# Performance work log

Measured on AMD Instinct MI355X. Metric: run time of the kernel, lower is better.

Reference implementation:

```python
import jax, jax.numpy as jnp
import numpy as np

C = 1024
H = 16
T = 2048
B = 2
EPS = 1e-5


def _layernorm(x, g, b):
    mu = jnp.mean(x, axis=-1, keepdims=True)
    var = jnp.mean(jnp.square(x - mu), axis=-1, keepdims=True)
    return (x - mu) * jax.lax.rsqrt(var + EPS) * g + b


def setup_inputs() -> dict:
    key = jax.random.key(0)
    ks = jax.random.split(key, 12)
    s = 1.0 / np.sqrt(C)
    inp = {
        "x": jax.random.normal(ks[0], (B, T, C), jnp.float32),
        "ln1_g": jnp.ones((C,), jnp.float32),
        "ln1_b": jnp.zeros((C,), jnp.float32),
        "Wq": jax.random.normal(ks[1], (C, C), jnp.float32) * s,
        "bq": jnp.zeros((C,), jnp.float32),
        "Wk": jax.random.normal(ks[2], (C, C), jnp.float32) * s,
        "bk": jnp.zeros((C,), jnp.float32),
        "Wv": jax.random.normal(ks[3], (C, C), jnp.float32) * s,
        "bv": jnp.zeros((C,), jnp.float32),
        "Wp": jax.random.normal(ks[4], (C, C), jnp.float32) * s,
        "bp": jnp.zeros((C,), jnp.float32),
        "ln2_g": jnp.ones((C,), jnp.float32),
        "ln2_b": jnp.zeros((C,), jnp.float32),
        "W1": jax.random.normal(ks[5], (C, 4 * C), jnp.float32) * s,
        "b1": jnp.zeros((4 * C,), jnp.float32),
        "W2": jax.random.normal(ks[6], (4 * C, C), jnp.float32) * (1.0 / np.sqrt(4 * C)),
        "b2": jnp.zeros((C,), jnp.float32),
    }
    return inp


def _block(x, ln1_g, ln1_b, Wq, bq, Wk, bk, Wv, bv, Wp, bp,
           ln2_g, ln2_b, W1, b1, W2, b2):
    b, t, c = x.shape
    hd = c // H
    h = _layernorm(x, ln1_g, ln1_b)
    q = (h @ Wq + bq).reshape(b, t, H, hd).transpose(0, 2, 1, 3)  # [B,H,T,hd]
    k = (h @ Wk + bk).reshape(b, t, H, hd).transpose(0, 2, 1, 3)
    v = (h @ Wv + bv).reshape(b, t, H, hd).transpose(0, 2, 1, 3)
    att = jnp.einsum("bhqd,bhkd->bhqk", q, k) * (1.0 / np.sqrt(hd))
    causal = jnp.tril(jnp.ones((t, t), bool))
    att = jnp.where(causal, att, -jnp.inf)
    att = jax.nn.softmax(att, axis=-1)
    y = jnp.einsum("bhqk,bhkd->bhqd", att, v)
    y = y.transpose(0, 2, 1, 3).reshape(b, t, c)
    x = x + (y @ Wp + bp)
    h2 = _layernorm(x, ln2_g, ln2_b)
    m = jax.nn.gelu(h2 @ W1 + b1, approximate=False)  # torch nn.GELU default = exact
    x = x + (m @ W2 + b2)
    return x


def reference(x, ln1_g, ln1_b, Wq, bq, Wk, bk, Wv, bv, Wp, bp,
              ln2_g, ln2_b, W1, b1, W2, b2):
    return _block(x, ln1_g, ln1_b, Wq, bq, Wk, bk, Wv, bv, Wp, bp,
                  ln2_g, ln2_b, W1, b1, W2, b2)
```

## Files before the change

### kernel.cpp

```cpp
#include <hip/hip_runtime.h>
#include <hip/hip_bf16.h>


#define TT 2048
#define CC 1024

typedef __attribute__((ext_vector_type(8))) short short8;
typedef __attribute__((ext_vector_type(4))) float floatx4;

__device__ __forceinline__ unsigned short f2bf(float f) {
    union { float f; unsigned u; } x; x.f = f;
    unsigned r = x.u + 0x7fff + ((x.u >> 16) & 1);
    return (unsigned short)(r >> 16);
}

__device__ __forceinline__ float fast_exp2(float x) {
#if __has_builtin(__builtin_amdgcn_exp2f)
    return __builtin_amdgcn_exp2f(x);
#else
    return exp2f(x);
#endif
}

__device__ __forceinline__ float fast_rcp(float x) {
#if __has_builtin(__builtin_amdgcn_rcpf)
    return __builtin_amdgcn_rcpf(x);
#else
    return 1.0f / x;
#endif
}

__device__ __forceinline__ float fast_gelu(float v) {
    float u = 0.79788456f * v + 0.035677408f * v * v * v;
    float e = fast_exp2(2.8853901f * u);
    return v - v * fast_rcp(e + 1.0f);
}

__device__ __forceinline__ void gld_lds16(const unsigned short* g, unsigned short* l) {
    __builtin_amdgcn_global_load_lds(
        (const __attribute__((address_space(1))) unsigned int*)g,
        (__attribute__((address_space(3))) unsigned int*)l, 16, 0, 0);
}

__global__ __launch_bounds__(256)
void prep_weights(const float* __restrict__ Wq, const float* __restrict__ Wk,
                  const float* __restrict__ Wv, const float* __restrict__ Wp,
                  const float* __restrict__ W1, const float* __restrict__ W2,
                  const float* __restrict__ bq, const float* __restrict__ bk,
                  const float* __restrict__ bv,
                  __hip_bfloat16* __restrict__ wqkvT, __hip_bfloat16* __restrict__ wpT,
                  __hip_bfloat16* __restrict__ w1T, __hip_bfloat16* __restrict__ w2T,
                  float* __restrict__ bqkv) {
    __shared__ float tile[32][33];
    int bid = blockIdx.x;
    int tid = threadIdx.x;
    if (bid >= 12288) {
#pragma unroll
        for (int it = 0; it < 12; ++it) {
            int i = it * 256 + tid;
            bqkv[i] = (i < 1024) ? bq[i] : (i < 2048) ? bk[i - 1024] : bv[i - 2048];
        }
        return;
    }
    const float* src; __hip_bfloat16* dst; int K, N, bxi, byi;
    if (bid < 4096) {
        int w = bid >> 10;
        src = (w == 0) ? Wq : (w == 1) ? Wk : (w == 2) ? Wv : Wp;
        dst = (w == 3) ? wpT : wqkvT + (size_t)w * 1024 * 1024;
        K = 1024; N = 1024;
        int r = bid & 1023; bxi = r & 31; byi = r >> 5;
    } else if (bid < 8192) {
        src = W1; dst = w1T; K = 1024; N = 4096;
        int r = bid - 4096; bxi = r & 127; byi = r >> 7;
    } else {
        src = W2; dst = w2T; K = 4096; N = 1024;
        int r = bid - 8192; bxi = r & 31; byi = r >> 5;
    }
    int tx = tid & 31, ty = tid >> 5;
    int n0 = bxi * 32, k0 = byi * 32;
#pragma unroll
    for (int i = 0; i < 4; ++i)
        tile[ty + i * 8][tx] = src[(size_t)(k0 + ty + i * 8) * N + n0 + tx];
    __syncthreads();
#pragma unroll
    for (int i = 0; i < 4; ++i)
        dst[(size_t)(n0 + ty + i * 8) * K + k0 + tx] = __float2bfloat16(tile[tx][ty + i * 8]);
}

__global__ __launch_bounds__(256)
void ln_kernel(const float* __restrict__ x, const float* __restrict__ g,
               const float* __restrict__ b, __hip_bfloat16* __restrict__ out) {
    int row = blockIdx.x;
    int tid = threadIdx.x;
    const float* xr = x + (size_t)row * CC;
    float4 v = *(const float4*)(xr + tid * 4);
    float s = v.x + v.y + v.z + v.w;
#pragma unroll
    for (int m = 1; m < 64; m <<= 1) s += __shfl_xor(s, m, 64);
    __shared__ float red[4], red2[4];
    int wv = tid >> 6;
    if ((tid & 63) == 0) red[wv] = s;
    __syncthreads();
    float mu = (red[0] + red[1] + red[2] + red[3]) * (1.0f / CC);
    float d0 = v.x - mu, d1 = v.y - mu, d2 = v.z - mu, d3 = v.w - mu;
    float s2 = d0 * d0 + d1 * d1 + d2 * d2 + d3 * d3;
#pragma unroll
    for (int m = 1; m < 64; m <<= 1) s2 += __shfl_xor(s2, m, 64);
    if ((tid & 63) == 0) red2[wv] = s2;
    __syncthreads();
    float var = (red2[0] + red2[1] + red2[2] + red2[3]) * (1.0f / CC);
    float rs = rsqrtf(var + 1e-5f);
    float4 gv = *(const float4*)(g + tid * 4);
    float4 bv = *(const float4*)(b + tid * 4);
    __hip_bfloat16* o = out + (size_t)row * CC + tid * 4;
    o[0] = __float2bfloat16(d0 * rs * gv.x + bv.x);
    o[1] = __float2bfloat16(d1 * rs * gv.y + bv.y);
    o[2] = __float2bfloat16(d2 * rs * gv.z + bv.z);
    o[3] = __float2bfloat16(d3 * rs * gv.w + bv.w);
}

#define BM 128
#define BK 64

template <int MODE, int TBN>
__global__ __launch_bounds__(256)
void gemm_bt(const unsigned short* __restrict__ A, const unsigned short* __restrict__ Bt,
             const float* __restrict__ bias, const float* __restrict__ res,
             void* __restrict__ out, unsigned short* __restrict__ vt,
             int M, int N, int K) {
    constexpr int IM = (TBN == 64) ? 2 : 4;
    __shared__ __align__(16) unsigned short As[BM * BK];
    __shared__ __align__(16) unsigned short Bs[TBN * BK];
    int tid = threadIdx.x;
    int lane = tid & 63;
    int wave = tid >> 6;
    int wm = (TBN == 64) ? wave * 32 : (wave >> 1) * 64;
    int wn = (TBN == 64) ? 0 : (wave & 1) * 64;
    int rowBase = blockIdx.x * BM;
    int colBase = blockIdx.y * TBN;
    int lr = lane & 15;
    int quad = lane >> 4;

    floatx4 acc[IM][4] = {};

    for (int k0 = 0; k0 < K; k0 += BK) {
#pragma unroll
        for (int hh = 0; hh < BM / 32; ++hh) {
            int s = tid + hh * 256;
            int r = s >> 3, p = s & 7;
            int c = p ^ (r & 7);
            gld_lds16(A + (size_t)(rowBase + r) * K + k0 + c * 8, As + (size_t)s * 8);
        }
#pragma unroll
        for (int hh = 0; hh < TBN / 32; ++hh) {
            int s = tid + hh * 256;
            int r = s >> 3, p = s & 7;
            int c = p ^ (r & 7);
            gld_lds16(Bt + (size_t)(colBase + r) * K + k0 + c * 8, Bs + (size_t)s * 8);
        }
        __syncthreads();
#pragma unroll
        for (int koi = 0; koi < 2; ++koi) {
            int ch = ((koi * 4 + quad) ^ (lr & 7)) * 8;
            short8 a[IM], b[4];
#pragma unroll
            for (int i = 0; i < IM; ++i)
                a[i] = *(const short8*)(As + (wm + i * 16 + lr) * BK + ch);
#pragma unroll
            for (int j = 0; j < 4; ++j)
                b[j] = *(const short8*)(Bs + (wn + j * 16 + lr) * BK + ch);
#pragma unroll
            for (int i = 0; i < IM; ++i)
#pragma unroll
                for (int j = 0; j < 4; ++j)
                    acc[i][j] = __builtin_amdgcn_mfma_f32_16x16x32_bf16(a[i], b[j], acc[i][j], 0, 0, 0);
        }
        __syncthreads();
    }

    if (MODE == 3 && colBase >= 2048) {
#pragma unroll
        for (int i = 0; i < IM; ++i) {
            int row0 = rowBase + wm + i * 16 + (lane >> 4) * 4;
            int bb = row0 >> 11, t0 = row0 & (TT - 1);
#pragma unroll
            for (int j = 0; j < 4; ++j) {
                int col = colBase + wn + j * 16 + (lane & 15);
                float bi = bias[col];
                int dg = col - 2048;
                int hh = dg >> 6, dd = dg & 63;
                ushort4 pk;
                pk.x = f2bf(acc[i][j][0] + bi);
                pk.y = f2bf(acc[i][j][1] + bi);
                pk.z = f2bf(acc[i][j][2] + bi);
                pk.w = f2bf(acc[i][j][3] + bi);
                *(ushort4*)(vt + ((size_t)(bb * 16 + hh) * 64 + dd) * TT + t0) = pk;
            }
        }
        return;
    }

    unsigned short* outb = (unsigned short*)out;
    float* outf = (float*)out;
#pragma unroll
    for (int i = 0; i < IM; ++i) {
        int row0 = rowBase + wm + i * 16 + (lane >> 4) * 4;
#pragma unroll
        for (int j = 0; j < 4; ++j) {
            int col = colBase + wn + j * 16 + (lane & 15);
            float bi = bias[col];
#pragma unroll
            for (int r = 0; r < 4; ++r) {
                size_t off = (size_t)(row0 + r) * N + col;
                float v = acc[i][j][r] + bi;
                if (MODE == 1) {
                    outf[off] = v + res[off];
                } else if (MODE == 2) {
                    outb[off] = f2bf(fast_gelu(v));
                } else {
                    outb[off] = f2bf(v);
                }
            }
        }
    }
}

__global__ __launch_bounds__(256)
void attn_mfma(const unsigned short* __restrict__ qkv,
               const unsigned short* __restrict__ vT,
               unsigned short* __restrict__ y) {
    __shared__ __align__(16) unsigned short Plds[4][32 * 72];
    __shared__ __align__(16) float cbuf[2][32][66];
    __shared__ float cltb[2][32];
    int wv = threadIdx.x >> 6, lane = threadIdx.x & 63;
    int quad = lane >> 4, l16 = lane & 15;
    int bx = blockIdx.x;
    int u = bx >> 5, bh = bx & 31;
    int t = wv >> 1, s = wv & 1;
    int qt = (31 - u) * 2 + t;
    int b = bh >> 4, h = bh & 15;

    const unsigned short* qb = qkv + (size_t)b * TT * 3072 + h * 64;
    const unsigned short* kb = qb + 1024;
    const unsigned short* vtb = vT + (size_t)bh * 64 * TT;
    unsigned short* Pw = Plds[wv];

    int q0 = qt * 32;
    short8 aq[2][2];
#pragma unroll
    for (int i = 0; i < 2; ++i)
#pragma unroll
        for (int c = 0; c < 2; ++c)
            aq[i][c] = *(const short8*)(qb + (size_t)(q0 + i * 16 + l16) * 3072 + c * 32 + quad * 8);

    short8 ones;
#pragma unroll
    for (int e = 0; e < 8; ++e) ones[e] = (short)0x3F80;

    floatx4 acc_o[2][4] = {};
    floatx4 lt[2] = {};

    const float k1 = 0.18033688f;
    const float k2 = 11.54156033f;

    int ntile = (qt >> 1) + 1;
    int nhalf = ntile >> 1;
    int ktbeg = s ? nhalf : 0;
    int ktend = s ? ntile : nhalf;

    for (int kt = ktbeg; kt < ktend; ++kt) {
        int k0 = kt * 64;
        short8 ck[4][2];
#pragma unroll
        for (int jt = 0; jt < 4; ++jt)
#pragma unroll
            for (int c = 0; c < 2; ++c)
                ck[jt][c] = *(const short8*)(kb + (size_t)(k0 + jt * 16 + l16) * 3072 + c * 32 + quad * 8);

        floatx4 sc[2][4] = {};
#pragma unroll
        for (int c = 0; c < 2; ++c)
#pragma unroll
            for (int i = 0; i < 2; ++i)
#pragma unroll
                for (int jt = 0; jt < 4; ++jt)
                    sc[i][jt] = __builtin_amdgcn_mfma_f32_16x16x32_bf16(aq[i][c], ck[jt][c], sc[i][jt], 0, 0, 0);

        if (kt == ntile - 1) {
#pragma unroll
            for (int i = 0; i < 2; ++i)
#pragma unroll
                for (int jt = 0; jt < 4; ++jt)
#pragma unroll
                    for (int r = 0; r < 4; ++r)
                        if (k0 + jt * 16 + l16 > q0 + i * 16 + quad * 4 + r) sc[i][jt][r] = -3.0e38f;
        }

#pragma unroll
        for (int i = 0; i < 2; ++i)
#pragma unroll
            for (int r = 0; r < 4; ++r) {
                int qrow = i * 16 + quad * 4 + r;
#pragma unroll
                for (int jt = 0; jt < 4; ++jt) {
                    float p = fast_exp2(fmaf(sc[i][jt][r], k1, -k2));
                    Pw[qrow * 72 + jt * 16 + l16] =
                        (unsigned short)(__float_as_uint(p) >> 16);
                }
            }

#pragma unroll
        for (int c = 0; c < 2; ++c) {
            short8 cv[4];
#pragma unroll
            for (int jd = 0; jd < 4; ++jd)
                cv[jd] = *(const short8*)(vtb + (size_t)(jd * 16 + l16) * TT + k0 + c * 32 + quad * 8);
#pragma unroll
            for (int i = 0; i < 2; ++i) {
                short8 ap = *(const short8*)(Pw + (i * 16 + l16) * 72 + c * 32 + quad * 8);
                lt[i] = __builtin_amdgcn_mfma_f32_16x16x32_bf16(ap, ones, lt[i], 0, 0, 0);
#pragma unroll
                for (int jd = 0; jd < 4; ++jd)
                    acc_o[i][jd] = __builtin_amdgcn_mfma_f32_16x16x32_bf16(ap, cv[jd], acc_o[i][jd], 0, 0, 0);
            }
        }
    }

    __syncthreads();
    if (s) {
#pragma unroll
        for (int i = 0; i < 2; ++i)
#pragma unroll
            for (int r = 0; r < 4; ++r) {
                int row = i * 16 + quad * 4 + r;
#pragma unroll
                for (int jd = 0; jd < 4; ++jd)
                    cbuf[t][row][jd * 16 + l16] = acc_o[i][jd][r];
                if (l16 == 0) cltb[t][row] = lt[i][r];
            }
    }
    __syncthreads();
    if (!s) {
#pragma unroll
        for (int i = 0; i < 2; ++i)
#pragma unroll
            for (int r = 0; r < 4; ++r) {
                int row = i * 16 + quad * 4 + r;
                float l2 = lt[i][r] + cltb[t][row];
                float rl = fast_rcp(l2);
                int grow = b * TT + q0 + row;
#pragma unroll
                for (int jd = 0; jd < 4; ++jd) {
                    float v = acc_o[i][jd][r] + cbuf[t][row][jd * 16 + l16];
                    y[(size_t)grow * CC + h * 64 + jd * 16 + l16] = f2bf(v * rl);
                }
            }
    }
}

extern "C" void kernel_launch(void* const* d_in, const int* in_sizes, int n_in,
                              void* d_out, int out_size, void* d_ws, size_t ws_size,
                              hipStream_t stream) {
    const float* x    = (const float*)d_in[0];
    const float* ln1g = (const float*)d_in[1];
    const float* ln1b = (const float*)d_in[2];
    const float* Wq   = (const float*)d_in[3];
    const float* bq   = (const float*)d_in[4];
    const float* Wk   = (const float*)d_in[5];
    const float* bk   = (const float*)d_in[6];
    const float* Wv   = (const float*)d_in[7];
    const float* bv   = (const float*)d_in[8];
    const float* Wp   = (const float*)d_in[9];
    const float* bp   = (const float*)d_in[10];
    const float* ln2g = (const float*)d_in[11];
    const float* ln2b = (const float*)d_in[12];
    const float* W1   = (const float*)d_in[13];
    const float* b1   = (const float*)d_in[14];
    const float* W2   = (const float*)d_in[15];
    const float* b2   = (const float*)d_in[16];

    const int M = 2 * TT;
    char* ws = (char*)d_ws;
    size_t off = 0;
    auto alloc = [&](size_t bytes) {
        char* p = ws + off;
        off += (bytes + 255) & ~(size_t)255;
        return p;
    };
    __hip_bfloat16* hb    = (__hip_bfloat16*)alloc((size_t)M * CC * 2);
    __hip_bfloat16* h2b   = (__hip_bfloat16*)alloc((size_t)M * CC * 2);
    unsigned short* yb    = (unsigned short*)alloc((size_t)M * CC * 2);
    __hip_bfloat16* wqkvT = (__hip_bfloat16*)alloc((size_t)3072 * CC * 2);
    __hip_bfloat16* wpT   = (__hip_bfloat16*)alloc((size_t)CC * CC * 2);
    __hip_bfloat16* w1T   = (__hip_bfloat16*)alloc((size_t)4096 * CC * 2);
    __hip_bfloat16* w2T   = (__hip_bfloat16*)alloc((size_t)CC * 4096 * 2);
    float*          bqkv  = (float*)alloc(3072 * 4);
    float*          x2    = (float*)alloc((size_t)M * CC * 4);
    unsigned short* qkv   = (unsigned short*)alloc((size_t)M * 3072 * 2);
    unsigned short* vT    = (unsigned short*)alloc((size_t)32 * 64 * TT * 2);
    unsigned short* mb    = (unsigned short*)alloc((size_t)M * 4096 * 2);
    (void)ws_size; (void)in_sizes; (void)n_in; (void)out_size;

    dim3 tb(256);
    prep_weights<<<12289, tb, 0, stream>>>(Wq, Wk, Wv, Wp, W1, W2, bq, bk, bv,
                                           wqkvT, wpT, w1T, w2T, bqkv);

    ln_kernel<<<M, 256, 0, stream>>>(x, ln1g, ln1b, hb);
    gemm_bt<3, 128><<<dim3(M / BM, 3072 / 128), tb, 0, stream>>>(
        (const unsigned short*)hb, (const unsigned short*)wqkvT, bqkv, nullptr, qkv, vT, M, 3072, 1024);
    attn_mfma<<<1024, tb, 0, stream>>>(qkv, vT, yb);
    gemm_bt<1, 64><<<dim3(M / BM, 1024 / 64), tb, 0, stream>>>(
        yb, (const unsigned short*)wpT, bp, x, x2, nullptr, M, 1024, 1024);
    ln_kernel<<<M, 256, 0, stream>>>(x2, ln2g, ln2b, h2b);
    gemm_bt<2, 128><<<dim3(M / BM, 4096 / 128), tb, 0, stream>>>(
        (const unsigned short*)h2b, (const unsigned short*)w1T, b1, nullptr, mb, nullptr, M, 4096, 1024);
    gemm_bt<1, 64><<<dim3(M / BM, 1024 / 64), tb, 0, stream>>>(
        mb, (const unsigned short*)w2T, b2, x2, (float*)d_out, nullptr, M, 1024, 4096);
}
```

Measured before the change: 378.6 us.

## Split attention key range across four waves per query tile, doubling grid

```diff
diff --git a/kernel.cpp b/kernel.cpp
--- a/kernel.cpp
+++ b/kernel.cpp
@@ -236,8 +236,8 @@
     int quad = lane >> 4, l16 = lane & 15;
     int bx = blockIdx.x;
     int u = bx >> 5, bh = bx & 31;
-    int t = wv >> 1, s = wv & 1;
-    int qt = (31 - u) * 2 + t;
+    int s = wv;
+    int qt = 63 - u;
     int b = bh >> 4, h = bh & 15;
 
     const unsigned short* qb = qkv + (size_t)b * TT * 3072 + h * 64;
@@ -264,9 +264,8 @@
     const float k2 = 11.54156033f;
 
     int ntile = (qt >> 1) + 1;
-    int nhalf = ntile >> 1;
-    int ktbeg = s ? nhalf : 0;
-    int ktend = s ? ntile : nhalf;
+    int ktbeg = (s * ntile) >> 2;
+    int ktend = ((s + 1) * ntile) >> 2;
 
     for (int kt = ktbeg; kt < ktend; ++kt) {
         int k0 = kt * 64;
@@ -327,7 +326,8 @@
     }
 
     __syncthreads();
-    if (s) {
+    if (s & 1) {
+        int cb = s >> 1;
 #pragma unroll
         for (int i = 0; i < 2; ++i)
 #pragma unroll
@@ -335,23 +335,50 @@
                 int row = i * 16 + quad * 4 + r;
 #pragma unroll
                 for (int jd = 0; jd < 4; ++jd)
-                    cbuf[t][row][jd * 16 + l16] = acc_o[i][jd][r];
-                if (l16 == 0) cltb[t][row] = lt[i][r];
-            }
-    }
-    __syncthreads();
-    if (!s) {
+                    cbuf[cb][row][jd * 16 + l16] = acc_o[i][jd][r];
+                if (l16 == 0) cltb[cb][row] = lt[i][r];
+            }
+    }
+    __syncthreads();
+    if (!(s & 1)) {
+        int cb = s >> 1;
 #pragma unroll
         for (int i = 0; i < 2; ++i)
 #pragma unroll
             for (int r = 0; r < 4; ++r) {
                 int row = i * 16 + quad * 4 + r;
-                float l2 = lt[i][r] + cltb[t][row];
+                lt[i][r] += cltb[cb][row];
+#pragma unroll
+                for (int jd = 0; jd < 4; ++jd)
+                    acc_o[i][jd][r] += cbuf[cb][row][jd * 16 + l16];
+            }
+    }
+    __syncthreads();
+    if (s == 2) {
+#pragma unroll
+        for (int i = 0; i < 2; ++i)
+#pragma unroll
+            for (int r = 0; r < 4; ++r) {
+                int row = i * 16 + quad * 4 + r;
+#pragma unroll
+                for (int jd = 0; jd < 4; ++jd)
+                    cbuf[0][row][jd * 16 + l16] = acc_o[i][jd][r];
+                if (l16 == 0) cltb[0][row] = lt[i][r];
+            }
+    }
+    __syncthreads();
+    if (s == 0) {
+#pragma unroll
+        for (int i = 0; i < 2; ++i)
+#pragma unroll
+            for (int r = 0; r < 4; ++r) {
+                int row = i * 16 + quad * 4 + r;
+                float l2 = lt[i][r] + cltb[0][row];
                 float rl = fast_rcp(l2);
                 int grow = b * TT + q0 + row;
 #pragma unroll
                 for (int jd = 0; jd < 4; ++jd) {
-                    float v = acc_o[i][jd][r] + cbuf[t][row][jd * 16 + l16];
+                    float v = acc_o[i][jd][r] + cbuf[0][row][jd * 16 + l16];
                     y[(size_t)grow * CC + h * 64 + jd * 16 + l16] = f2bf(v * rl);
                 }
             }
@@ -408,7 +435,7 @@
     ln_kernel<<<M, 256, 0, stream>>>(x, ln1g, ln1b, hb);
     gemm_bt<3, 128><<<dim3(M / BM, 3072 / 128), tb, 0, stream>>>(
         (const unsigned short*)hb, (const unsigned short*)wqkvT, bqkv, nullptr, qkv, vT, M, 3072, 1024);
-    attn_mfma<<<1024, tb, 0, stream>>>(qkv, vT, yb);
+    attn_mfma<<<2048, tb, 0, stream>>>(qkv, vT, yb);
     gemm_bt<1, 64><<<dim3(M / BM, 1024 / 64), tb, 0, stream>>>(
         yb, (const unsigned short*)wpT, bp, x, x2, nullptr, M, 1024, 1024);
     ln_kernel<<<M, 256, 0, stream>>>(x2, ln2g, ln2b, h2b);
```

Measured after the change: 378.8 us. Within noise of the previous version (+0.1%).

## Pair long and short causal query tiles per block to balance attention work

Applied to the files above, without the earlier changes.

```diff
diff --git a/kernel.cpp b/kernel.cpp
--- a/kernel.cpp
+++ b/kernel.cpp
@@ -236,98 +236,112 @@
     int quad = lane >> 4, l16 = lane & 15;
     int bx = blockIdx.x;
     int u = bx >> 5, bh = bx & 31;
-    int t = wv >> 1, s = wv & 1;
-    int qt = (31 - u) * 2 + t;
     int b = bh >> 4, h = bh & 15;
+    int qtA = 63 - u, qtB = u;
+    int nA = (qtA >> 1) + 1, nB = (qtB >> 1) + 1;
+
+    {
+        float* cz = &cbuf[0][0][0];
+        for (int i = threadIdx.x; i < 2 * 32 * 66; i += 256) cz[i] = 0.0f;
+        if (threadIdx.x < 64) (&cltb[0][0])[threadIdx.x] = 0.0f;
+    }
+    __syncthreads();
 
     const unsigned short* qb = qkv + (size_t)b * TT * 3072 + h * 64;
     const unsigned short* kb = qb + 1024;
     const unsigned short* vtb = vT + (size_t)bh * 64 * TT;
     unsigned short* Pw = Plds[wv];
 
-    int q0 = qt * 32;
-    short8 aq[2][2];
-#pragma unroll
-    for (int i = 0; i < 2; ++i)
-#pragma unroll
-        for (int c = 0; c < 2; ++c)
-            aq[i][c] = *(const short8*)(qb + (size_t)(q0 + i * 16 + l16) * 3072 + c * 32 + quad * 8);
-
     short8 ones;
 #pragma unroll
     for (int e = 0; e < 8; ++e) ones[e] = (short)0x3F80;
-
-    floatx4 acc_o[2][4] = {};
-    floatx4 lt[2] = {};
 
     const float k1 = 0.18033688f;
     const float k2 = 11.54156033f;
 
-    int ntile = (qt >> 1) + 1;
-    int nhalf = ntile >> 1;
-    int ktbeg = s ? nhalf : 0;
-    int ktend = s ? ntile : nhalf;
-
-    for (int kt = ktbeg; kt < ktend; ++kt) {
-        int k0 = kt * 64;
-        short8 ck[4][2];
-#pragma unroll
-        for (int jt = 0; jt < 4; ++jt)
+    int fbeg = (33 * wv) >> 2, fend = (33 * (wv + 1)) >> 2;
+
+    for (int seg = 0; seg < 2; ++seg) {
+        int t, sb, se;
+        if (seg == 0) {
+            if (fbeg < nA) { t = 0; sb = fbeg; se = (fend < nA) ? fend : nA; }
+            else           { t = 1; sb = fbeg - nA; se = fend - nA; }
+        } else {
+            if (fbeg < nA && fend > nA) { t = 1; sb = 0; se = fend - nA; }
+            else break;
+        }
+        int qt = t ? qtB : qtA;
+        int ntile = t ? nB : nA;
+        int q0 = qt * 32;
+
+        short8 aq[2][2];
+#pragma unroll
+        for (int i = 0; i < 2; ++i)
 #pragma unroll
             for (int c = 0; c < 2; ++c)
-                ck[jt][c] = *(const short8*)(kb + (size_t)(k0 + jt * 16 + l16) * 3072 + c * 32 + quad * 8);
-
-        floatx4 sc[2][4] = {};
-#pragma unroll
-        for (int c = 0; c < 2; ++c)
+                aq[i][c] = *(const short8*)(qb + (size_t)(q0 + i * 16 + l16) * 3072 + c * 32 + quad * 8);
+
+        floatx4 acc_o[2][4] = {};
+        floatx4 lt[2] = {};
+
+        for (int kt = sb; kt < se; ++kt) {
+            int k0 = kt * 64;
+            short8 ck[4][2];
+#pragma unroll
+            for (int jt = 0; jt < 4; ++jt)
+#pragma unroll
+                for (int c = 0; c < 2; ++c)
+                    ck[jt][c] = *(const short8*)(kb + (size_t)(k0 + jt * 16 + l16) * 3072 + c * 32 + quad * 8);
+
+            floatx4 sc[2][4] = {};
+#pragma unroll
+            for (int c = 0; c < 2; ++c)
+#pragma unroll
+                for (int i = 0; i < 2; ++i)
+#pragma unroll
+                    for (int jt = 0; jt < 4; ++jt)
+                        sc[i][jt] = __builtin_amdgcn_mfma_f32_16x16x32_bf16(aq[i][c], ck[jt][c], sc[i][jt], 0, 0, 0);
+
+            if (kt == ntile - 1) {
+#pragma unroll
+                for (int i = 0; i < 2; ++i)
+#pragma unroll
+                    for (int jt = 0; jt < 4; ++jt)
+#pragma unroll
+                        for (int r = 0; r < 4; ++r)
+                            if (k0 + jt * 16 + l16 > q0 + i * 16 + quad * 4 + r) sc[i][jt][r] = -3.0e38f;
+            }
+
 #pragma unroll
             for (int i = 0; i < 2; ++i)
 #pragma unroll
-                for (int jt = 0; jt < 4; ++jt)
-                    sc[i][jt] = __builtin_amdgcn_mfma_f32_16x16x32_bf16(aq[i][c], ck[jt][c], sc[i][jt], 0, 0, 0);
-
-        if (kt == ntile - 1) {
-#pragma unroll
-            for (int i = 0; i < 2; ++i)
-#pragma unroll
-                for (int jt = 0; jt < 4; ++jt)
-#pragma unroll
-                    for (int r = 0; r < 4; ++r)
-                        if (k0 + jt * 16 + l16 > q0 + i * 16 + quad * 4 + r) sc[i][jt][r] = -3.0e38f;
-        }
-
-#pragma unroll
-        for (int i = 0; i < 2; ++i)
-#pragma unroll
-            for (int r = 0; r < 4; ++r) {
-                int qrow = i * 16 + quad * 4 + r;
-#pragma unroll
-                for (int jt = 0; jt < 4; ++jt) {
-                    float p = fast_exp2(fmaf(sc[i][jt][r], k1, -k2));
-                    Pw[qrow * 72 + jt * 16 + l16] =
-                        (unsigned short)(__float_as_uint(p) >> 16);
+                for (int r = 0; r < 4; ++r) {
+                    int qrow = i * 16 + quad * 4 + r;
+#pragma unroll
+                    for (int jt = 0; jt < 4; ++jt) {
+                        float p = fast_exp2(fmaf(sc[i][jt][r], k1, -k2));
+                        Pw[qrow * 72 + jt * 16 + l16] =
+                            (unsigned short)(__float_as_uint(p) >> 16);
+                    }
                 }
-            }
-
-#pragma unroll
-        for (int c = 0; c < 2; ++c) {
-            short8 cv[4];
-#pragma unroll
-            for (int jd = 0; jd < 4; ++jd)
-                cv[jd] = *(const short8*)(vtb + (size_t)(jd * 16 + l16) * TT + k0 + c * 32 + quad * 8);
-#pragma unroll
-            for (int i = 0; i < 2; ++i) {
-                short8 ap = *(const short8*)(Pw + (i * 16 + l16) * 72 + c * 32 + quad * 8);
-                lt[i] = __builtin_amdgcn_mfma_f32_16x16x32_bf16(ap, ones, lt[i], 0, 0, 0);
+
+#pragma unroll
+            for (int c = 0; c < 2; ++c) {
+                short8 cv[4];
 #pragma unroll
                 for (int jd = 0; jd < 4; ++jd)
-                    acc_o[i][jd] = __builtin_amdgcn_mfma_f32_16x16x32_bf16(ap, cv[jd], acc_o[i][jd], 0, 0, 0);
-            }
-        }
-    }
-
-    __syncthreads();
-    if (s) {
+                    cv[jd] = *(const short8*)(vtb + (size_t)(jd * 16 + l16) * TT + k0 + c * 32 + quad * 8);
+#pragma unroll
+                for (int i = 0; i < 2; ++i) {
+                    short8 ap = *(const short8*)(Pw + (i * 16 + l16) * 72 + c * 32 + quad * 8);
+                    lt[i] = __builtin_amdgcn_mfma_f32_16x16x32_bf16(ap, ones, lt[i], 0, 0, 0);
+#pragma unroll
+                    for (int jd = 0; jd < 4; ++jd)
+                        acc_o[i][jd] = __builtin_amdgcn_mfma_f32_16x16x32_bf16(ap, cv[jd], acc_o[i][jd], 0, 0, 0);
+                }
+            }
+        }
+
 #pragma unroll
         for (int i = 0; i < 2; ++i)
 #pragma unroll
@@ -335,23 +349,26 @@
                 int row = i * 16 + quad * 4 + r;
 #pragma unroll
                 for (int jd = 0; jd < 4; ++jd)
-                    cbuf[t][row][jd * 16 + l16] = acc_o[i][jd][r];
-                if (l16 == 0) cltb[t][row] = lt[i][r];
-            }
-    }
+                    atomicAdd(&cbuf[t][row][jd * 16 + l16], acc_o[i][jd][r]);
+                if (l16 == 0) atomicAdd(&cltb[t][row], lt[i][r]);
+            }
+    }
+
     __syncthreads();
-    if (!s) {
+    if (wv < 2) {
+        int t = wv;
+        int qt = t ? qtB : qtA;
+        int q0 = qt * 32;
 #pragma unroll
         for (int i = 0; i < 2; ++i)
 #pragma unroll
             for (int r = 0; r < 4; ++r) {
                 int row = i * 16 + quad * 4 + r;
-                float l2 = lt[i][r] + cltb[t][row];
-                float rl = fast_rcp(l2);
+                float rl = fast_rcp(cltb[t][row]);
                 int grow = b * TT + q0 + row;
 #pragma unroll
                 for (int jd = 0; jd < 4; ++jd) {
-                    float v = acc_o[i][jd][r] + cbuf[t][row][jd * 16 + l16];
+                    float v = cbuf[t][row][jd * 16 + l16];
                     y[(size_t)grow * CC + h * 64 + jd * 16 + l16] = f2bf(v * rl);
                 }
             }
```

After: 416.1 us. 1.1x slower.
